# Performance work log

Hardware: AMD Instinct MI355X
Metric: run time of the kernel (lower is better)

The kernel has to match this reference:

```python
import jax, jax.numpy as jnp
import numpy as np
import math


def setup_inputs() -> dict:
    key = jax.random.key(0)
    kq, kk, kv, km = jax.random.split(key, 4)
    B, Lq, Lk, D = 4, 4096, 4096, 64
    queries = jax.random.normal(kq, (B, Lq, D), dtype=jnp.float32)
    keys = jax.random.normal(kk, (B, Lk, D), dtype=jnp.float32)
    values = jax.random.normal(kv, (B, Lk, D), dtype=jnp.float32)
    masks = jax.random.randint(km, (B, Lk), 0, 2, dtype=jnp.int32)
    return {"queries": queries, "keys": keys, "values": values, "masks": masks}


def reference(queries, keys, values, masks):
    # scale = sqrt(d_k) (self.scale is None)
    d_k = queries.shape[-1]
    scale = math.sqrt(d_k)
    # scores: [B, Lq, Lk]
    scores = jnp.einsum('bqd,bkd->bqk', queries, keys) / jnp.asarray(scale, queries.dtype)
    # key-padding mask [B, Lk] -> broadcast over Lq; masked positions -> -inf
    neg_inf = jnp.asarray(float('-inf'), scores.dtype)
    scores = jnp.where(masks[:, None, :] == 0, neg_inf, scores)
    attn = jax.nn.softmax(scores, axis=-1)  # dropout p=0 -> identity
    return jnp.einsum('bqk,bkd->bqd', attn, values)
```

## Files before the change

kernel.cpp:

```cpp
#include <hip/hip_runtime.h>


#define B_N    4
#define L      4096
#define DH     64
#define TILE_K 64
#define KPAD   72
#define SPLIT  8
#define SLAB   (L / SPLIT)
#define TILES  (SLAB / TILE_K)
#define QSCALE 0.18033688f

typedef unsigned short ushort8_ma __attribute__((ext_vector_type(8), may_alias));
typedef unsigned short ushort4_ma __attribute__((ext_vector_type(4), may_alias));
typedef float          f32x4_ma   __attribute__((ext_vector_type(4), may_alias));
typedef short          short8     __attribute__((ext_vector_type(8)));
typedef float          f32x16     __attribute__((ext_vector_type(16)));
typedef unsigned int   uint2_ev   __attribute__((ext_vector_type(2)));

union v8cast  { ushort8_ma u; short8 s; };
union pk4cast { unsigned int u[4]; short8 s; };

static __device__ __forceinline__ short8 ld8(const unsigned short* p) {
    v8cast x; x.u = *(const ushort8_ma*)p; return x.s;
}
static __device__ __forceinline__ unsigned short bf16rne(float f) {
    union { float f; unsigned u; } x; x.f = f;
    unsigned r = x.u + 0x7fffu + ((x.u >> 16) & 1u);
    return (unsigned short)(r >> 16);
}
static __device__ __forceinline__ float bf16tof(unsigned short u) {
    union { unsigned u; float f; } x; x.u = (unsigned)u << 16; return x.f;
}
static __device__ __forceinline__ float fast_exp2(float x) {
    return __builtin_amdgcn_exp2f(x);
}
static __device__ __forceinline__ unsigned cvt_pk_bf16(float lo, float hi) {
    unsigned r;
    asm("v_cvt_pk_bf16_f32 %0, %1, %2" : "=v"(r) : "v"(lo), "v"(hi));
    return r;
}
static __device__ __forceinline__ short8 build_P(const f32x16& p, int b0) {
    unsigned A0 = cvt_pk_bf16(p[b0 + 0], p[b0 + 1]);
    unsigned A1 = cvt_pk_bf16(p[b0 + 2], p[b0 + 3]);
    unsigned B0 = cvt_pk_bf16(p[b0 + 4], p[b0 + 5]);
    unsigned B1 = cvt_pk_bf16(p[b0 + 6], p[b0 + 7]);
    uint2_ev r02 = __builtin_amdgcn_permlane32_swap(A0, B0, false, false);
    uint2_ev r13 = __builtin_amdgcn_permlane32_swap(A1, B1, false, false);
    pk4cast P;
    P.u[0] = r02[0]; P.u[1] = r13[0];
    P.u[2] = r02[1]; P.u[3] = r13[1];
    return P.s;
}

__global__ __launch_bounds__(256)
void prepass3(const float* __restrict__ Q, const float* __restrict__ K,
              const float* __restrict__ V, const int* __restrict__ M,
              unsigned short* __restrict__ Qb, unsigned short* __restrict__ Kb,
              unsigned short* __restrict__ Vt)
{
    __shared__ unsigned short t[64][20];
    const int b  = blockIdx.y;
    const int r0 = blockIdx.x * 16;
    const size_t base = ((size_t)b * L + r0) * DH;

    {
        int i = threadIdx.x;
        int row = i >> 4, d0 = (i & 15) * 4;
        size_t off = base + (size_t)row * DH + d0;
        f32x4_ma q = *(const f32x4_ma*)(Q + off);
        f32x4_ma k = *(const f32x4_ma*)(K + off);
        f32x4_ma v = *(const f32x4_ma*)(V + off);
        const float zf = (M[(size_t)b * L + r0 + row] == 0) ? 0.f : 1.f;
        ushort4_ma qo, ko;
        #pragma unroll
        for (int j = 0; j < 4; ++j) {
            qo[j] = bf16rne(q[j] * QSCALE);
            ko[j] = bf16rne(k[j] * zf);
            t[d0 + j][row] = bf16rne(v[j] * zf);
        }
        *(ushort4_ma*)(Qb + off) = qo;
        *(ushort4_ma*)(Kb + off) = ko;
    }
    __syncthreads();
    {
        int i = threadIdx.x;
        int d = i >> 2, k4 = (i & 3) * 4;
        ushort4_ma vo = { t[d][k4], t[d][k4 + 1], t[d][k4 + 2], t[d][k4 + 3] };
        *(ushort4_ma*)(Vt + ((size_t)b * DH + d) * L + r0 + k4) = vo;
    }
}

__global__ __launch_bounds__(256, 2)
void fa_split64(const unsigned short* __restrict__ Qb,
                const unsigned short* __restrict__ Kb,
                const unsigned short* __restrict__ Vt,
                const int*            __restrict__ Mk,
                unsigned short* __restrict__ ACCp, float* __restrict__ Lp)
{
    __shared__ unsigned short Kl[TILE_K * KPAD];
    __shared__ unsigned short Vl[DH * KPAD];
    __shared__ int            cntw[4];

    const int tid  = threadIdx.x;
    const int wave = tid >> 6;
    const int lane = tid & 63;
    const int l32  = lane & 31;
    const int hw   = lane >> 5;

    const int b      = blockIdx.y & (B_N - 1);
    const int slab   = blockIdx.y >> 2;
    const int qblock = blockIdx.x * 256;
    const int kbase  = slab * SLAB;
    const int qbase  = qblock + wave * 64;

    short8 q00, q01, q02, q03, q10, q11, q12, q13;
    {
        const unsigned short* qp0 = Qb + ((size_t)b * L + qbase + l32) * DH + hw * 8;
        const unsigned short* qp1 = qp0 + 32 * DH;
        q00 = ld8(qp0);      q01 = ld8(qp0 + 16);
        q02 = ld8(qp0 + 32); q03 = ld8(qp0 + 48);
        q10 = ld8(qp1);      q11 = ld8(qp1 + 16);
        q12 = ld8(qp1 + 32); q13 = ld8(qp1 + 48);
    }

    const unsigned short* Kbb = Kb + (size_t)b * L * DH;
    const unsigned short* Vtb = Vt + (size_t)b * DH * L;
    const int*            Mb  = Mk + (size_t)b * L;

    const int c1 = tid + 256;
    const int r0 = tid >> 3, d0 = (tid & 7) * 8;
    const int r1 = c1 >> 3,  d1 = (c1 & 7) * 8;

    ushort8_ma kr0, kr1, vr0, vr1;
    int mr_unused = 0; (void)mr_unused;

    kr0 = *(const ushort8_ma*)(Kbb + (size_t)(kbase + r0) * DH + d0);
    kr1 = *(const ushort8_ma*)(Kbb + (size_t)(kbase + r1) * DH + d1);
    vr0 = *(const ushort8_ma*)(Vtb + (size_t)r0 * L + kbase + d0);
    vr1 = *(const ushort8_ma*)(Vtb + (size_t)r1 * L + kbase + d1);
    const int m0 = Mb[kbase + 2 * tid];
    const int m1 = Mb[kbase + 2 * tid + 1];
    *(ushort8_ma*)(&Kl[r0 * KPAD + d0]) = kr0;
    *(ushort8_ma*)(&Kl[r1 * KPAD + d1]) = kr1;
    *(ushort8_ma*)(&Vl[r0 * KPAD + d0]) = vr0;
    *(ushort8_ma*)(&Vl[r1 * KPAD + d1]) = vr1;
    {
        unsigned long long bm0 = __ballot(m0 == 0);
        unsigned long long bm1 = __ballot(m1 == 0);
        if (lane == 0) cntw[wave] = __popcll(bm0) + __popcll(bm1);
    }
    __syncthreads();

    f32x16 a00 = {0}, a01 = {0}, a10 = {0}, a11 = {0};
    float rA0 = 0.f, rA1 = 0.f, rA2 = 0.f, rA3 = 0.f;
    float rB0 = 0.f, rB1 = 0.f, rB2 = 0.f, rB3 = 0.f;

    for (int t = 0; t < TILES; ++t) {
        if (t < TILES - 1) {
            const int k0n = kbase + (t + 1) * TILE_K;
            kr0 = *(const ushort8_ma*)(Kbb + (size_t)(k0n + r0) * DH + d0);
            kr1 = *(const ushort8_ma*)(Kbb + (size_t)(k0n + r1) * DH + d1);
            vr0 = *(const ushort8_ma*)(Vtb + (size_t)r0 * L + k0n + d0);
            vr1 = *(const ushort8_ma*)(Vtb + (size_t)r1 * L + k0n + d1);
        }

        #pragma unroll
        for (int g = 0; g < 2; ++g) {
            const unsigned short* kp = &Kl[(g * 32 + l32) * KPAD + hw * 8];
            short8 aK0 = ld8(kp);
            short8 aK1 = ld8(kp + 16);
            short8 aK2 = ld8(kp + 32);
            short8 aK3 = ld8(kp + 48);

            f32x16 s0 = {0}, s1 = {0};
            s0 = __builtin_amdgcn_mfma_f32_32x32x16_bf16(aK0, q00, s0, 0, 0, 0);
            s1 = __builtin_amdgcn_mfma_f32_32x32x16_bf16(aK0, q10, s1, 0, 0, 0);
            s0 = __builtin_amdgcn_mfma_f32_32x32x16_bf16(aK1, q01, s0, 0, 0, 0);
            s1 = __builtin_amdgcn_mfma_f32_32x32x16_bf16(aK1, q11, s1, 0, 0, 0);
            s0 = __builtin_amdgcn_mfma_f32_32x32x16_bf16(aK2, q02, s0, 0, 0, 0);
            s1 = __builtin_amdgcn_mfma_f32_32x32x16_bf16(aK2, q12, s1, 0, 0, 0);
            s0 = __builtin_amdgcn_mfma_f32_32x32x16_bf16(aK3, q03, s0, 0, 0, 0);
            s1 = __builtin_amdgcn_mfma_f32_32x32x16_bf16(aK3, q13, s1, 0, 0, 0);

            f32x16 p0, p1;
            #pragma unroll
            for (int r = 0; r < 16; r += 4) {
                p0[r + 0] = fast_exp2(s0[r + 0]); rA0 += p0[r + 0];
                p0[r + 1] = fast_exp2(s0[r + 1]); rA1 += p0[r + 1];
                p0[r + 2] = fast_exp2(s0[r + 2]); rA2 += p0[r + 2];
                p0[r + 3] = fast_exp2(s0[r + 3]); rA3 += p0[r + 3];
            }
            #pragma unroll
            for (int r = 0; r < 16; r += 4) {
                p1[r + 0] = fast_exp2(s1[r + 0]); rB0 += p1[r + 0];
                p1[r + 1] = fast_exp2(s1[r + 1]); rB1 += p1[r + 1];
                p1[r + 2] = fast_exp2(s1[r + 2]); rB2 += p1[r + 2];
                p1[r + 3] = fast_exp2(s1[r + 3]); rB3 += p1[r + 3];
            }
            #pragma unroll
            for (int h = 0; h < 2; ++h) {
                const int kk = 2 * g + h;
                const unsigned short* vp = &Vl[l32 * KPAD + kk * 16 + hw * 8];
                short8 bV0 = ld8(vp);
                short8 bV1 = ld8(vp + 32 * KPAD);
                short8 P0 = build_P(p0, 8 * h);
                a00 = __builtin_amdgcn_mfma_f32_32x32x16_bf16(P0, bV0, a00, 0, 0, 0);
                a01 = __builtin_amdgcn_mfma_f32_32x32x16_bf16(P0, bV1, a01, 0, 0, 0);
                short8 P1 = build_P(p1, 8 * h);
                a10 = __builtin_amdgcn_mfma_f32_32x32x16_bf16(P1, bV0, a10, 0, 0, 0);
                a11 = __builtin_amdgcn_mfma_f32_32x32x16_bf16(P1, bV1, a11, 0, 0, 0);
            }
        }

        __syncthreads();
        if (t < TILES - 1) {
            *(ushort8_ma*)(&Kl[r0 * KPAD + d0]) = kr0;
            *(ushort8_ma*)(&Kl[r1 * KPAD + d1]) = kr1;
            *(ushort8_ma*)(&Vl[r0 * KPAD + d0]) = vr0;
            *(ushort8_ma*)(&Vl[r1 * KPAD + d1]) = vr1;
            __syncthreads();
        }
    }

    float rsA = (rA0 + rA1) + (rA2 + rA3);
    float rsB = (rB0 + rB1) + (rB2 + rB3);
    rsA += __shfl_xor(rsA, 32);
    rsB += __shfl_xor(rsB, 32);
    const float scnt = (float)(cntw[0] + cntw[1] + cntw[2] + cntw[3]);
    const size_t pbase = ((size_t)(slab * B_N + b)) * L;
    #pragma unroll
    for (int reg = 0; reg < 16; ++reg) {
        int row = (reg & 3) + 8 * (reg >> 2) + 4 * hw;
        unsigned short* ap0 = ACCp + (pbase + qbase + row) * DH;
        unsigned short* ap1 = ACCp + (pbase + qbase + 32 + row) * DH;
        ap0[l32]      = bf16rne(a00[reg]);
        ap0[32 + l32] = bf16rne(a01[reg]);
        ap1[l32]      = bf16rne(a10[reg]);
        ap1[32 + l32] = bf16rne(a11[reg]);
    }
    if (hw == 0) {
        Lp[pbase + qbase + l32]      = rsA - scnt;
        Lp[pbase + qbase + 32 + l32] = rsB - scnt;
    }
}

__global__ __launch_bounds__(256)
void fa_combine(const unsigned short* __restrict__ ACCp,
                const float* __restrict__ Lp, float* __restrict__ O)
{
    const int b    = blockIdx.y;
    const int qrow = blockIdx.x * 4 + (threadIdx.x >> 6);
    const int d    = threadIdx.x & 63;

    float lsum = 0.f, o = 0.f;
    #pragma unroll
    for (int s = 0; s < SPLIT; ++s) {
        lsum += Lp[((size_t)(s * B_N + b)) * L + qrow];
        o    += bf16tof(ACCp[(((size_t)(s * B_N + b)) * L + qrow) * DH + d]);
    }
    O[((size_t)b * L + qrow) * DH + d] = o / fmaxf(lsum, 1e-20f);
}

#define TK  64
#define RW  4
#define RB  16
#define KST 67

__global__ __launch_bounds__(256)
void fa_scalar(const float* __restrict__ Q, const float* __restrict__ K,
               const float* __restrict__ V, const int* __restrict__ Mk,
               float* __restrict__ O)
{
    __shared__ float Kt[TK][KST];
    __shared__ float Vts[DH][KST];
    __shared__ float Qs[RB][DH];
    __shared__ float Ps[4][RW][TK];
    __shared__ float Bs[TK];

    const int tid = threadIdx.x, w = tid >> 6, lane = tid & 63;
    const int b = blockIdx.y, row0 = blockIdx.x * RB;

    for (int i = tid; i < RB * DH; i += 256) {
        int r = i >> 6, d = i & 63;
        Qs[r][d] = Q[((size_t)b * L + row0 + r) * DH + d];
    }
    float m[RW], l[RW], acc[RW];
    #pragma unroll
    for (int rr = 0; rr < RW; ++rr) { m[rr] = -1e30f; l[rr] = 0.f; acc[rr] = 0.f; }

    for (int k0 = 0; k0 < L; k0 += TK) {
        __syncthreads();
        for (int i = tid; i < TK * DH; i += 256) {
            int key = i >> 6, d = i & 63;
            Kt[key][d]  = K[((size_t)b * L + k0 + key) * DH + d];
            Vts[d][key] = V[((size_t)b * L + k0 + key) * DH + d];
        }
        if (tid < TK) Bs[tid] = (Mk[(size_t)b * L + k0 + tid] == 0) ? -1e30f : 0.f;
        __syncthreads();
        float s[RW];
        #pragma unroll
        for (int rr = 0; rr < RW; ++rr) s[rr] = 0.f;
        for (int d4 = 0; d4 < DH; d4 += 4) {
            float kv[4];
            #pragma unroll
            for (int j = 0; j < 4; ++j) kv[j] = Kt[lane][d4 + j];
            #pragma unroll
            for (int rr = 0; rr < RW; ++rr)
                #pragma unroll
                for (int j = 0; j < 4; ++j)
                    s[rr] += Qs[w * RW + rr][d4 + j] * kv[j];
        }
        float alpha[RW];
        #pragma unroll
        for (int rr = 0; rr < RW; ++rr) {
            float sv = s[rr] * 0.125f + Bs[lane];
            float t = sv;
            #pragma unroll
            for (int off = 1; off < 64; off <<= 1) t = fmaxf(t, __shfl_xor(t, off));
            float mnew = fmaxf(m[rr], t);
            alpha[rr] = __expf(fminf(m[rr] - mnew, 0.f));
            float p = __expf(fminf(sv - mnew, 0.f));
            Ps[w][rr][lane] = p;
            float su = p;
            #pragma unroll
            for (int off = 1; off < 64; off <<= 1) su += __shfl_xor(su, off);
            l[rr] = l[rr] * alpha[rr] + su;
            m[rr] = mnew;
        }
        __syncthreads();
        #pragma unroll
        for (int rr = 0; rr < RW; ++rr) acc[rr] *= alpha[rr];
        for (int k4 = 0; k4 < TK; k4 += 4) {
            float vv[4];
            #pragma unroll
            for (int j = 0; j < 4; ++j) vv[j] = Vts[lane][k4 + j];
            #pragma unroll
            for (int rr = 0; rr < RW; ++rr)
                #pragma unroll
                for (int j = 0; j < 4; ++j)
                    acc[rr] += Ps[w][rr][k4 + j] * vv[j];
        }
    }
    #pragma unroll
    for (int rr = 0; rr < RW; ++rr) {
        int row = row0 + w * RW + rr;
        O[((size_t)b * L + row) * DH + lane] = acc[rr] / fmaxf(l[rr], 1e-20f);
    }
}

extern "C" void kernel_launch(void* const* d_in, const int* in_sizes, int n_in,
                              void* d_out, int out_size, void* d_ws, size_t ws_size,
                              hipStream_t stream) {
    const float* Q = (const float*)d_in[0];
    const float* K = (const float*)d_in[1];
    const float* V = (const float*)d_in[2];
    const int*   M = (const int*)d_in[3];
    float*       O = (float*)d_out;

    const size_t elems     = (size_t)B_N * L * DH;
    const size_t bf16_need = elems * 2 * 3;
    const size_t acc_elems = (size_t)SPLIT * B_N * L * DH;
    const size_t ml_elems  = (size_t)SPLIT * B_N * L;
    const size_t full_need = bf16_need + acc_elems * 2 + ml_elems * 4;

    unsigned short* Qb = (unsigned short*)d_ws;
    unsigned short* Kb = Qb + elems;
    unsigned short* Vt = Kb + elems;

    if (ws_size >= full_need) {
        unsigned short* ACCp = Vt + elems;
        float*          Lp   = (float*)(ACCp + acc_elems);

        prepass3<<<dim3(L / 16, B_N), dim3(256), 0, stream>>>(Q, K, V, M, Qb, Kb, Vt);
        fa_split64<<<dim3(L / 256, B_N * SPLIT), dim3(256), 0, stream>>>(
            Qb, Kb, Vt, M, ACCp, Lp);
        fa_combine<<<dim3(L / 4, B_N), dim3(256), 0, stream>>>(ACCp, Lp, O);
    } else {
        fa_scalar<<<dim3(L / RB, B_N), dim3(256), 0, stream>>>(Q, K, V, M, O);
    }
}
```

Baseline: 93.29 us.

## Double-buffer K/V LDS tiles with two-deep register prefetch and single barrier

The K/V shared-memory tiles are now double-buffered, so the next tile is written into the other buffer while the current one is consumed. This cuts synchronisation to one barrier per tile instead of two. Global loads are issued two tiles ahead through two alternating register sets, and the fully unrolled tile loop lets the buffer choice resolve at compile time. The cost is double the LDS footprint and extra registers, which could pressure occupancy under the 2-blocks-per-CU launch bound.

```diff
diff --git a/kernel.cpp b/kernel.cpp
--- a/kernel.cpp
+++ b/kernel.cpp
@@ -92,14 +92,14 @@
 }
 
 __global__ __launch_bounds__(256, 2)
-void fa_split64(const unsigned short* __restrict__ Qb,
-                const unsigned short* __restrict__ Kb,
-                const unsigned short* __restrict__ Vt,
-                const int*            __restrict__ Mk,
-                unsigned short* __restrict__ ACCp, float* __restrict__ Lp)
+void fa_pipe64(const unsigned short* __restrict__ Qb,
+               const unsigned short* __restrict__ Kb,
+               const unsigned short* __restrict__ Vt,
+               const int*            __restrict__ Mk,
+               unsigned short* __restrict__ ACCp, float* __restrict__ Lp)
 {
-    __shared__ unsigned short Kl[TILE_K * KPAD];
-    __shared__ unsigned short Vl[DH * KPAD];
+    __shared__ unsigned short Kl[2][TILE_K * KPAD];
+    __shared__ unsigned short Vl[2][DH * KPAD];
     __shared__ int            cntw[4];
 
     const int tid  = threadIdx.x;
@@ -132,19 +132,36 @@
     const int r0 = tid >> 3, d0 = (tid & 7) * 8;
     const int r1 = c1 >> 3,  d1 = (c1 & 7) * 8;
 
-    ushort8_ma kr0, kr1, vr0, vr1;
-    int mr_unused = 0; (void)mr_unused;
-
-    kr0 = *(const ushort8_ma*)(Kbb + (size_t)(kbase + r0) * DH + d0);
-    kr1 = *(const ushort8_ma*)(Kbb + (size_t)(kbase + r1) * DH + d1);
-    vr0 = *(const ushort8_ma*)(Vtb + (size_t)r0 * L + kbase + d0);
-    vr1 = *(const ushort8_ma*)(Vtb + (size_t)r1 * L + kbase + d1);
+    ushort8_ma kA0, kA1, vA0, vA1, kB0, kB1, vB0, vB1;
+
+#define LOADSET(SK0, SK1, SV0, SV1, TAU) do {                                  \
+        const int k0n_ = kbase + (TAU) * TILE_K;                               \
+        SK0 = *(const ushort8_ma*)(Kbb + (size_t)(k0n_ + r0) * DH + d0);       \
+        SK1 = *(const ushort8_ma*)(Kbb + (size_t)(k0n_ + r1) * DH + d1);       \
+        SV0 = *(const ushort8_ma*)(Vtb + (size_t)r0 * L + k0n_ + d0);          \
+        SV1 = *(const ushort8_ma*)(Vtb + (size_t)r1 * L + k0n_ + d1);          \
+    } while (0)
+
+#define WRITESET(BUF, SK0, SK1, SV0, SV1) do {                                 \
+        *(ushort8_ma*)(&Kl[BUF][r0 * KPAD + d0]) = SK0;                        \
+        *(ushort8_ma*)(&Kl[BUF][r1 * KPAD + d1]) = SK1;                        \
+        *(ushort8_ma*)(&Vl[BUF][r0 * KPAD + d0]) = SV0;                        \
+        *(ushort8_ma*)(&Vl[BUF][r1 * KPAD + d1]) = SV1;                        \
+    } while (0)
+
+#define LBAR() do {                                                            \
+        asm volatile("s_waitcnt lgkmcnt(0)" ::: "memory");                     \
+        __builtin_amdgcn_sched_barrier(0);                                     \
+        __builtin_amdgcn_s_barrier();                                          \
+        __builtin_amdgcn_sched_barrier(0);                                     \
+    } while (0)
+
+    LOADSET(kA0, kA1, vA0, vA1, 0);
+    LOADSET(kB0, kB1, vB0, vB1, 1);
     const int m0 = Mb[kbase + 2 * tid];
     const int m1 = Mb[kbase + 2 * tid + 1];
-    *(ushort8_ma*)(&Kl[r0 * KPAD + d0]) = kr0;
-    *(ushort8_ma*)(&Kl[r1 * KPAD + d1]) = kr1;
-    *(ushort8_ma*)(&Vl[r0 * KPAD + d0]) = vr0;
-    *(ushort8_ma*)(&Vl[r1 * KPAD + d1]) = vr1;
+    WRITESET(0, kA0, kA1, vA0, vA1);
+    LOADSET(kA0, kA1, vA0, vA1, 2);
     {
         unsigned long long bm0 = __ballot(m0 == 0);
         unsigned long long bm1 = __ballot(m1 == 0);
@@ -156,18 +173,13 @@
     float rA0 = 0.f, rA1 = 0.f, rA2 = 0.f, rA3 = 0.f;
     float rB0 = 0.f, rB1 = 0.f, rB2 = 0.f, rB3 = 0.f;
 
+    #pragma unroll
     for (int t = 0; t < TILES; ++t) {
-        if (t < TILES - 1) {
-            const int k0n = kbase + (t + 1) * TILE_K;
-            kr0 = *(const ushort8_ma*)(Kbb + (size_t)(k0n + r0) * DH + d0);
-            kr1 = *(const ushort8_ma*)(Kbb + (size_t)(k0n + r1) * DH + d1);
-            vr0 = *(const ushort8_ma*)(Vtb + (size_t)r0 * L + k0n + d0);
-            vr1 = *(const ushort8_ma*)(Vtb + (size_t)r1 * L + k0n + d1);
-        }
+        const int cur = t & 1;
 
         #pragma unroll
         for (int g = 0; g < 2; ++g) {
-            const unsigned short* kp = &Kl[(g * 32 + l32) * KPAD + hw * 8];
+            const unsigned short* kp = &Kl[cur][(g * 32 + l32) * KPAD + hw * 8];
             short8 aK0 = ld8(kp);
             short8 aK1 = ld8(kp + 16);
             short8 aK2 = ld8(kp + 32);
@@ -201,7 +213,7 @@
             #pragma unroll
             for (int h = 0; h < 2; ++h) {
                 const int kk = 2 * g + h;
-                const unsigned short* vp = &Vl[l32 * KPAD + kk * 16 + hw * 8];
+                const unsigned short* vp = &Vl[cur][l32 * KPAD + kk * 16 + hw * 8];
                 short8 bV0 = ld8(vp);
                 short8 bV1 = ld8(vp + 32 * KPAD);
                 short8 P0 = build_P(p0, 8 * h);
@@ -213,15 +225,20 @@
             }
         }
 
-        __syncthreads();
         if (t < TILES - 1) {
-            *(ushort8_ma*)(&Kl[r0 * KPAD + d0]) = kr0;
-            *(ushort8_ma*)(&Kl[r1 * KPAD + d1]) = kr1;
-            *(ushort8_ma*)(&Vl[r0 * KPAD + d0]) = vr0;
-            *(ushort8_ma*)(&Vl[r1 * KPAD + d1]) = vr1;
-            __syncthreads();
-        }
-    }
+            const int nxt = cur ^ 1;
+            if ((t + 1) & 1) WRITESET(nxt, kB0, kB1, vB0, vB1);
+            else             WRITESET(nxt, kA0, kA1, vA0, vA1);
+            LBAR();
+            if (t + 3 < TILES) {
+                if ((t + 3) & 1) LOADSET(kB0, kB1, vB0, vB1, t + 3);
+                else             LOADSET(kA0, kA1, vA0, vA1, t + 3);
+            }
+        }
+    }
+#undef LOADSET
+#undef WRITESET
+#undef LBAR
 
     float rsA = (rA0 + rA1) + (rA2 + rA3);
     float rsB = (rB0 + rB1) + (rB2 + rB3);
@@ -373,7 +390,7 @@
         float*          Lp   = (float*)(ACCp + acc_elems);
 
         prepass3<<<dim3(L / 16, B_N), dim3(256), 0, stream>>>(Q, K, V, M, Qb, Kb, Vt);
-        fa_split64<<<dim3(L / 256, B_N * SPLIT), dim3(256), 0, stream>>>(
+        fa_pipe64<<<dim3(L / 256, B_N * SPLIT), dim3(256), 0, stream>>>(
             Qb, Kb, Vt, M, ACCp, Lp);
         fa_combine<<<dim3(L / 4, B_N), dim3(256), 0, stream>>>(ACCp, Lp, O);
     } else {
```

New measurement: 94.05 us. No clear change (+0.8%).
